# Kernel tuning notes

Measured on AMD Instinct MI355X. Metric: run time of the kernel, lower is better.

Reference implementation:

```python
import jax, jax.numpy as jnp
import numpy as np

M, L, Q = 512, 256, 21


def setup_inputs() -> dict:
    key = jax.random.key(0)
    k1, k2, k3 = jax.random.split(key, 3)
    # one-hot encoded sequences (M, L, q)
    X_idx = jax.random.randint(k1, (M, L), 0, Q)
    X_oh = jax.nn.one_hot(X_idx, Q, dtype=jnp.float32)
    h_pos = 0.01 * jax.random.normal(k2, (L, Q), dtype=jnp.float32)
    J = 0.01 * jax.random.normal(k3, (L, L, Q, Q), dtype=jnp.float32)
    return {"X_oh": X_oh, "h_pos": h_pos, "J": J}


def reference(X_oh, h_pos, J):
    # z[m,i,a] = h[i,a] + sum_{j<i} sum_b J[i,j,b,a] * X[m,j,b]
    # (matches torch einsum 'mpq,pqr->mpr' over tril-gathered blocks)
    L_, q_ = h_pos.shape
    i_idx, j_idx = jnp.tril_indices(L_, k=-1)          # (P,), strictly lower, i sorted
    J_blocks = J[i_idx, j_idx]                          # (P, q, q)
    X_blocks = X_oh[:, j_idx]                           # (M, P, q)
    contrib = jnp.einsum('mpb,pba->mpa', X_blocks, J_blocks)  # (M, P, q)
    # scatter-add contributions to their target position i (sorted segments)
    agg = jax.ops.segment_sum(
        jnp.swapaxes(contrib, 0, 1),                    # (P, M, q)
        i_idx, num_segments=L_, indices_are_sorted=True
    )                                                   # (L, M, q)
    return h_pos[None, :, :] + jnp.swapaxes(agg, 0, 1)  # (M, L, q)
```

## Files before the change

### kernel.cpp

```cpp
#include <hip/hip_runtime.h>

#define L_DIM 256
#define M_DIM 512
#define Q_DIM 21
#define BLKB   1764
#define SLOT   1920
#define IDXOFF 1792
#define NBUF   4
#define DEPTH  3

#define GLD(src, dst, sz) __builtin_amdgcn_global_load_lds( \
    (const __attribute__((address_space(1))) void*)(src),   \
    (__attribute__((address_space(3))) void*)(dst), sz, 0, 0)

__global__ __launch_bounds__(64) void ardca_prep(const float* __restrict__ X_oh,
                                                 unsigned short* __restrict__ Xt) {
  int w = blockIdx.x;
  int lane = threadIdx.x;
  const float* base = X_oh + (size_t)w * (64 * Q_DIM);
  int rowbase = w * 64;
#pragma unroll 4
  for (int p = 0; p < 22; ++p) {
    int f = p * 63 + lane;
    float v = (lane < 63 && f < 1344) ? base[f] : 0.0f;
    unsigned long long mask = __ballot(v > 0.5f);
    if (lane < 3) {
      int rloc = 3 * p + lane;
      if (rloc < 64) {
        unsigned int bits = (unsigned int)((mask >> (21 * lane)) & 0x1FFFFFu);
        int x = bits ? __builtin_ctz(bits) : 0;
        int rr = rowbase + rloc;
        int m = rr >> 8, j = rr & 255;
        Xt[j * M_DIM + m] = (unsigned short)(x * 84);
      }
    }
  }
}

template <int USE_XT>
__global__ __launch_bounds__(64) void ardca_main(const float* __restrict__ Jm,
                                                 const float* __restrict__ h,
                                                 const unsigned short* __restrict__ Xt,
                                                 const float* __restrict__ X_oh,
                                                 float* __restrict__ out) {
  alignas(16) __shared__ char lds[NBUF * SLOT];
  int b = blockIdx.x;
  int c = b & 7;
  int r = b >> 3;
  int mg = r & 15;
  int i = ((31 - (r >> 4)) << 3) | c;
  int lane = threadIdx.x;
  int ml = lane & 31;
  int ah = lane >> 5;
  int m = mg * 32 + ml;

  const char* Jrow = (const char*)Jm + (size_t)i * (256ull * BLKB);
  const char* XtB  = (const char*)Xt;

  float acc[12];
  const float* hp = h + i * Q_DIM + ah * 12;
#pragma unroll
  for (int k = 0; k < 12; ++k) acc[k] = (ah == 0 || k < 9) ? hp[k] : 0.0f;

  auto STAGE = [&](int j) {
    char* buf = lds + (j & (NBUF - 1)) * SLOT;
    unsigned bb = (unsigned)j * BLKB;
    const char* src = Jrow + (bb & ~15u);
    GLD(src + lane * 16, buf, 16);
    if (lane < 48) GLD(src + 1024 + lane * 16, buf + 1024, 16);
    if (USE_XT) {
      if (lane < 16) GLD(XtB + j * 1024 + mg * 64 + lane * 4, buf + IDXOFF, 4);
    }
  };

  auto CONSUME = [&](int j) {
    const char* buf = lds + (j & (NBUF - 1)) * SLOT;
    int off;
    if (USE_XT) {
      off = *(const unsigned short*)(buf + IDXOFF + 2 * ml);
    } else {
      const float* p = X_oh + ((size_t)m * L_DIM + j) * Q_DIM;
      int x = 0;
#pragma unroll
      for (int a = 0; a < Q_DIM; ++a) x = (p[a] > 0.5f) ? a : x;
      off = x * 84;
    }
    const float* row = (const float*)(buf + ((j & 3) << 2) + off) + ah * 12;
#pragma unroll
    for (int k = 0; k < 12; ++k) acc[k] += row[k];
  };

  int P = (i < DEPTH) ? i : DEPTH;
  for (int j = 0; j < P; ++j) STAGE(j);
  int jt = i - DEPTH; if (jt < 0) jt = 0;

#pragma unroll 1
  for (int j = 0; j < jt; ++j) {
    STAGE(j + DEPTH);
    if (USE_XT) {
      asm volatile("s_waitcnt vmcnt(9)" ::: "memory");
    } else {
      asm volatile("s_waitcnt vmcnt(0)" ::: "memory");
    }
    __builtin_amdgcn_sched_barrier(0);
    CONSUME(j);
  }
  asm volatile("s_waitcnt vmcnt(0)" ::: "memory");
  __builtin_amdgcn_sched_barrier(0);
#pragma unroll 1
  for (int j = jt; j < i; ++j) CONSUME(j);

  float* o = out + ((size_t)m * L_DIM + i) * Q_DIM + ah * 12;
  if (ah == 0) {
#pragma unroll
    for (int k = 0; k < 12; ++k) o[k] = acc[k];
  } else {
#pragma unroll
    for (int k = 0; k < 9; ++k) o[k] = acc[k];
  }
}

extern "C" void kernel_launch(void* const* d_in, const int* in_sizes, int n_in,
                              void* d_out, int out_size, void* d_ws, size_t ws_size,
                              hipStream_t stream) {
  const float* X_oh = (const float*)d_in[0];
  const float* h    = (const float*)d_in[1];
  const float* Jm   = (const float*)d_in[2];
  float* out        = (float*)d_out;
  unsigned short* Xt = (unsigned short*)d_ws;

  if (ws_size >= (size_t)M_DIM * L_DIM * sizeof(unsigned short)) {
    ardca_prep<<<2048, 64, 0, stream>>>(X_oh, Xt);
    ardca_main<1><<<4096, 64, 0, stream>>>(Jm, h, Xt, X_oh, out);
  } else {
    ardca_main<0><<<4096, 64, 0, stream>>>(Jm, h, Xt, X_oh, out);
  }
}
```

Measured before the change: 236.5 us.

## Share each staged J block across eight wavefronts in 512-thread workgroups

Replaces 4096 single-wave blocks, each covering one row i and 32 sequences, with 512 workgroups of 512 threads, each covering one i and 256 sequences. Each J(i,j) block and its index slice are staged into LDS once and read by all eight waves, so J is fetched from global memory far fewer times. Work is assigned so that long and short rows are interleaved across the grid. The cost is a workgroup barrier on every j step and a deeper six-slot LDS ring, and coarser blocks that leave the triangular load less evenly balanced.

```diff
diff --git a/kernel.cpp b/kernel.cpp
--- a/kernel.cpp
+++ b/kernel.cpp
@@ -1,13 +1,11 @@
 #include <hip/hip_runtime.h>
 
-#define L_DIM 256
-#define M_DIM 512
 #define Q_DIM 21
-#define BLKB   1764
-#define SLOT   1920
-#define IDXOFF 1792
-#define NBUF   4
-#define DEPTH  3
+#define BLKB  1764
+#define WINB  1792
+#define SLOT  2304
+#define NBUF  6
+#define DEPTH 3
 
 #define GLD(src, dst, sz) __builtin_amdgcn_global_load_lds( \
     (const __attribute__((address_space(1))) void*)(src),   \
@@ -17,75 +15,76 @@
                                                  unsigned short* __restrict__ Xt) {
   int w = blockIdx.x;
   int lane = threadIdx.x;
-  const float* base = X_oh + (size_t)w * (64 * Q_DIM);
-  int rowbase = w * 64;
-#pragma unroll 4
-  for (int p = 0; p < 22; ++p) {
+  const float* base = X_oh + (size_t)w * (32 * Q_DIM);
+  int rowbase = w * 32;
+#pragma unroll
+  for (int p = 0; p < 11; ++p) {
     int f = p * 63 + lane;
-    float v = (lane < 63 && f < 1344) ? base[f] : 0.0f;
+    float v = (lane < 63 && f < 672) ? base[f] : 0.0f;
     unsigned long long mask = __ballot(v > 0.5f);
     if (lane < 3) {
       int rloc = 3 * p + lane;
-      if (rloc < 64) {
+      if (rloc < 32) {
         unsigned int bits = (unsigned int)((mask >> (21 * lane)) & 0x1FFFFFu);
         int x = bits ? __builtin_ctz(bits) : 0;
         int rr = rowbase + rloc;
         int m = rr >> 8, j = rr & 255;
-        Xt[j * M_DIM + m] = (unsigned short)(x * 84);
+        Xt[j * 512 + m] = (unsigned short)(x * 84);
       }
     }
   }
 }
 
 template <int USE_XT>
-__global__ __launch_bounds__(64) void ardca_main(const float* __restrict__ Jm,
-                                                 const float* __restrict__ h,
-                                                 const unsigned short* __restrict__ Xt,
-                                                 const float* __restrict__ X_oh,
-                                                 float* __restrict__ out) {
+__global__ __launch_bounds__(512, 4) void ardca_main(const float* __restrict__ Jm,
+                                                     const float* __restrict__ h,
+                                                     const unsigned short* __restrict__ Xt,
+                                                     const float* __restrict__ X_oh,
+                                                     float* __restrict__ out) {
   alignas(16) __shared__ char lds[NBUF * SLOT];
   int b = blockIdx.x;
-  int c = b & 7;
-  int r = b >> 3;
-  int mg = r & 15;
-  int i = ((31 - (r >> 4)) << 3) | c;
-  int lane = threadIdx.x;
-  int ml = lane & 31;
-  int ah = lane >> 5;
-  int m = mg * 32 + ml;
+  int i, mh;
+  if (b < 256) { i = b; mh = 0; }
+  else { int x = b - 256; i = 248 - (x & ~7) + (x & 7); mh = 1; }
+  int tid = threadIdx.x;
+  int ml = tid & 255;
+  int ah = tid >> 8;
+  int m = mh * 256 + ml;
 
   const char* Jrow = (const char*)Jm + (size_t)i * (256ull * BLKB);
   const char* XtB  = (const char*)Xt;
 
+  const float* hp = h + i * Q_DIM + ah * 12;
   float acc[12];
-  const float* hp = h + i * Q_DIM + ah * 12;
 #pragma unroll
-  for (int k = 0; k < 12; ++k) acc[k] = (ah == 0 || k < 9) ? hp[k] : 0.0f;
+  for (int k = 0; k < 12; ++k)
+    acc[k] = (k < 9 || ah == 0) ? hp[k] : 0.0f;
 
   auto STAGE = [&](int j) {
-    char* buf = lds + (j & (NBUF - 1)) * SLOT;
+    char* buf = lds + (j % NBUF) * SLOT;
     unsigned bb = (unsigned)j * BLKB;
     const char* src = Jrow + (bb & ~15u);
-    GLD(src + lane * 16, buf, 16);
-    if (lane < 48) GLD(src + 1024 + lane * 16, buf + 1024, 16);
+    if (tid < 112) GLD(src + tid * 16, buf + tid * 16, 16);
     if (USE_XT) {
-      if (lane < 16) GLD(XtB + j * 1024 + mg * 64 + lane * 4, buf + IDXOFF, 4);
+      if (tid >= 128 && tid < 160)
+        GLD(XtB + j * 1024 + mh * 512 + (tid - 128) * 16,
+            buf + WINB + (tid - 128) * 16, 16);
     }
   };
 
   auto CONSUME = [&](int j) {
-    const char* buf = lds + (j & (NBUF - 1)) * SLOT;
+    const char* buf = lds + (j % NBUF) * SLOT;
     int off;
     if (USE_XT) {
-      off = *(const unsigned short*)(buf + IDXOFF + 2 * ml);
+      off = *(const unsigned short*)(buf + WINB + 2 * ml);
     } else {
-      const float* p = X_oh + ((size_t)m * L_DIM + j) * Q_DIM;
+      const float* p = X_oh + ((size_t)m * 256 + j) * Q_DIM;
       int x = 0;
 #pragma unroll
       for (int a = 0; a < Q_DIM; ++a) x = (p[a] > 0.5f) ? a : x;
       off = x * 84;
     }
-    const float* row = (const float*)(buf + ((j & 3) << 2) + off) + ah * 12;
+    const float* row = (const float*)(buf + ((j & 3) << 2) + off + ah * 48);
 #pragma unroll
     for (int k = 0; k < 12; ++k) acc[k] += row[k];
   };
@@ -97,20 +96,19 @@
 #pragma unroll 1
   for (int j = 0; j < jt; ++j) {
     STAGE(j + DEPTH);
-    if (USE_XT) {
-      asm volatile("s_waitcnt vmcnt(9)" ::: "memory");
-    } else {
-      asm volatile("s_waitcnt vmcnt(0)" ::: "memory");
-    }
+    if (USE_XT) asm volatile("s_waitcnt vmcnt(3)" ::: "memory");
+    else        asm volatile("s_waitcnt vmcnt(0)" ::: "memory");
     __builtin_amdgcn_sched_barrier(0);
+    __builtin_amdgcn_s_barrier();
     CONSUME(j);
   }
   asm volatile("s_waitcnt vmcnt(0)" ::: "memory");
   __builtin_amdgcn_sched_barrier(0);
+  __builtin_amdgcn_s_barrier();
 #pragma unroll 1
   for (int j = jt; j < i; ++j) CONSUME(j);
 
-  float* o = out + ((size_t)m * L_DIM + i) * Q_DIM + ah * 12;
+  float* o = out + ((size_t)m * 256 + i) * Q_DIM + ah * 12;
   if (ah == 0) {
 #pragma unroll
     for (int k = 0; k < 12; ++k) o[k] = acc[k];
@@ -129,10 +127,10 @@
   float* out        = (float*)d_out;
   unsigned short* Xt = (unsigned short*)d_ws;
 
-  if (ws_size >= (size_t)M_DIM * L_DIM * sizeof(unsigned short)) {
-    ardca_prep<<<2048, 64, 0, stream>>>(X_oh, Xt);
-    ardca_main<1><<<4096, 64, 0, stream>>>(Jm, h, Xt, X_oh, out);
+  if (ws_size >= 262144) {
+    ardca_prep<<<4096, 64, 0, stream>>>(X_oh, Xt);
+    ardca_main<1><<<512, 512, 0, stream>>>(Jm, h, Xt, X_oh, out);
   } else {
-    ardca_main<0><<<4096, 64, 0, stream>>>(Jm, h, Xt, X_oh, out);
+    ardca_main<0><<<512, 512, 0, stream>>>(Jm, h, Xt, X_oh, out);
   }
 }
```

Result: faster. 223.0 us (-5.7%).
